# Optimization experiments

Measured on AMD Instinct MI355X. Metric: run time of the kernel, lower is better.

## Reference

```python
import jax, jax.numpy as jnp
import numpy as np

N_USERS = 100000
N_ITEMS = 50000
N_NODES = N_USERS + N_ITEMS
EMB = 64
N_LAYERS = 2
N_EDGES = 4000000
LN_EPS = 1e-5


def setup_inputs() -> dict:
    key = jax.random.key(0)
    ks = jax.random.split(key, 16)
    d = {}
    d['user_emb'] = jax.random.normal(ks[0], (N_USERS, EMB), jnp.float32) * 0.1
    d['item_emb'] = jax.random.normal(ks[1], (N_ITEMS, EMB), jnp.float32) * 0.1
    d['modal_feat0'] = jax.random.normal(ks[2], (N_ITEMS, 768), jnp.float32)
    d['modal_feat1'] = jax.random.normal(ks[3], (N_ITEMS, 384), jnp.float32)
    d['modal_feat2'] = jax.random.normal(ks[4], (N_USERS, 128), jnp.float32)
    for m, fdim in enumerate([768, 384, 128]):
        d[f'enc_W{m}'] = jax.random.normal(ks[5 + m], (fdim, EMB), jnp.float32) / np.sqrt(fdim)
        d[f'enc_b{m}'] = jnp.zeros((EMB,), jnp.float32)
        d[f'enc_g{m}'] = jnp.ones((EMB,), jnp.float32)
        d[f'enc_be{m}'] = jnp.zeros((EMB,), jnp.float32)
    d['attn_W1'] = jax.random.normal(ks[8], (2 * EMB, EMB), jnp.float32) / np.sqrt(2 * EMB)
    d['attn_b1'] = jnp.zeros((EMB,), jnp.float32)
    d['attn_W2'] = jax.random.normal(ks[9], (EMB, 3), jnp.float32) / np.sqrt(EMB)
    d['attn_b2'] = jnp.zeros((3,), jnp.float32)
    # symmetric-normalized-ish positive edge weights, COO edge list
    d['adj_vals'] = jax.random.uniform(ks[10], (N_EDGES,), jnp.float32) * 0.05
    d['adj_rows'] = jax.random.randint(ks[11], (N_EDGES,), 0, N_NODES, jnp.int32)
    d['adj_cols'] = jax.random.randint(ks[12], (N_EDGES,), 0, N_NODES, jnp.int32)
    return d


def _layernorm(h, g, b):
    mu = h.mean(-1, keepdims=True)
    var = ((h - mu) ** 2).mean(-1, keepdims=True)
    return (h - mu) * jax.lax.rsqrt(var + LN_EPS) * g + b


def _encode(x, W, b, g, be):
    # Linear -> LayerNorm -> LeakyReLU(0.2); Dropout is identity at inference
    return jax.nn.leaky_relu(_layernorm(x @ W + b, g, be), 0.2)


def reference(user_emb, item_emb, modal_feat0, modal_feat1, modal_feat2,
              enc_W0, enc_b0, enc_g0, enc_be0,
              enc_W1, enc_b1, enc_g1, enc_be1,
              enc_W2, enc_b2, enc_g2, enc_be2,
              attn_W1, attn_b1, attn_W2, attn_b2,
              adj_vals, adj_rows, adj_cols):
    # item-level modalities
    m0 = _encode(modal_feat0, enc_W0, enc_b0, enc_g0, enc_be0)        # [I, D]
    m1 = _encode(modal_feat1, enc_W1, enc_b1, enc_g1, enc_be1)        # [I, D]
    # user-level modality: mean over users, broadcast to items
    um = _encode(modal_feat2, enc_W2, enc_b2, enc_g2, enc_be2)        # [U, D]
    m2 = jnp.broadcast_to(um.mean(0, keepdims=True), (N_ITEMS, EMB))  # [I, D]
    item_modal = jnp.stack([m0, m1, m2], axis=1)                      # [I, 3, D]

    # modal attention from (mean user emb, item emb)
    u_mean = jnp.broadcast_to(user_emb.mean(0, keepdims=True), (N_ITEMS, EMB))
    att_in = jnp.concatenate([u_mean, item_emb], axis=1)              # [I, 2D]
    w = jax.nn.softmax(jnp.tanh(att_in @ attn_W1 + attn_b1) @ attn_W2 + attn_b2, axis=-1)  # [I, 3]
    item_weighted = jnp.einsum('imd,im->id', item_modal, w)

    all_emb = jnp.concatenate([user_emb, item_emb + item_weighted], axis=0)  # [N, D]

    def spmm(e):
        return jax.ops.segment_sum(adj_vals[:, None] * e[adj_cols], adj_rows,
                                   num_segments=N_NODES)

    acc = all_emb
    e = all_emb
    for _ in range(N_LAYERS):
        e = spmm(e)
        acc = acc + e
    out = acc / (N_LAYERS + 1)
    return out[:N_USERS], out[N_USERS:]
```

## Files before the change

kernel.cpp:

```cpp
#include <hip/hip_runtime.h>
#include <cstdint>

#define N_USERS 100000
#define N_ITEMS 50000
#define N_NODES (N_USERS + N_ITEMS)
#define EMB 64
#define N_EDGES 4000000
#define LN_EPS 1e-5f

#define NBKT 586
#define C_BLOCKS 1024
#define EPB 3907
#define BCAP 7680
#define ENC128_BLOCKS 1563
#define ENC_ITEM_BLOCKS 782
#define UPREP_BLOCKS 512

#define K1_SMEM 37056

__device__ __forceinline__ float b2f(unsigned short h) {
    return __uint_as_float((unsigned)h << 16);
}
__device__ __forceinline__ unsigned short f2b(float f) {
    unsigned u = __float_as_uint(f);
    u += 0x7FFFu + ((u >> 16) & 1u);
    return (unsigned short)(u >> 16);
}
__device__ __forceinline__ uint2 pack4(float a, float b, float c, float d) {
    return make_uint2((unsigned)f2b(a) | ((unsigned)f2b(b) << 16),
                      (unsigned)f2b(c) | ((unsigned)f2b(d) << 16));
}

template<int WRITE_OUT>
__device__ __forceinline__ void enc_body(
    int blk, char* smem, const float* __restrict__ X, const float* __restrict__ W,
    const float* __restrict__ bb, const float* __restrict__ gg,
    const float* __restrict__ be, float* __restrict__ out,
    float* __restrict__ colsum, int K, int R)
{
    float (*sXT)[68] = reinterpret_cast<float(*)[68]>(smem);
    float (*sW)[64] = reinterpret_cast<float(*)[64]>(smem + 8704);
    float* scs = reinterpret_cast<float*>(smem + 8704 + 8192);

    int tid = threadIdx.x;
    int tx = tid & 15;
    int ty = tid >> 4;
    int rbase = blk * 64;

    int xr = tid >> 2;
    int xc = (tid & 3) * 8;
    int wr = tid >> 3;
    int wc = (tid & 7) * 8;

    int gxrow = rbase + xr; if (gxrow >= R) gxrow = R - 1;
    const float* xsrc = X + (size_t)gxrow * K + xc;

    float4 bv = *reinterpret_cast<const float4*>(&bb[tx * 4]);
    float4 gv = *reinterpret_cast<const float4*>(&gg[tx * 4]);
    float4 bev = *reinterpret_cast<const float4*>(&be[tx * 4]);

    float acc[4][4];
    #pragma unroll
    for (int i = 0; i < 4; ++i) {
        acc[i][0] = bv.x; acc[i][1] = bv.y; acc[i][2] = bv.z; acc[i][3] = bv.w;
    }

    for (int kc = 0; kc < K; kc += 32) {
        float4 a0 = *reinterpret_cast<const float4*>(xsrc + kc);
        float4 a1 = *reinterpret_cast<const float4*>(xsrc + kc + 4);
        float4 w0 = *reinterpret_cast<const float4*>(&W[(size_t)(kc + wr) * EMB + wc]);
        float4 w1 = *reinterpret_cast<const float4*>(&W[(size_t)(kc + wr) * EMB + wc + 4]);
        __syncthreads();
        sXT[xc + 0][xr] = a0.x; sXT[xc + 1][xr] = a0.y;
        sXT[xc + 2][xr] = a0.z; sXT[xc + 3][xr] = a0.w;
        sXT[xc + 4][xr] = a1.x; sXT[xc + 5][xr] = a1.y;
        sXT[xc + 6][xr] = a1.z; sXT[xc + 7][xr] = a1.w;
        *reinterpret_cast<float4*>(&sW[wr][wc]) = w0;
        *reinterpret_cast<float4*>(&sW[wr][wc + 4]) = w1;
        __syncthreads();
        #pragma unroll
        for (int k = 0; k < 32; ++k) {
            float4 xv = *reinterpret_cast<const float4*>(&sXT[k][ty * 4]);
            float4 wv = *reinterpret_cast<const float4*>(&sW[k][tx * 4]);
            float xs[4] = {xv.x, xv.y, xv.z, xv.w};
            float wsv[4] = {wv.x, wv.y, wv.z, wv.w};
            #pragma unroll
            for (int i = 0; i < 4; ++i)
                #pragma unroll
                for (int j = 0; j < 4; ++j)
                    acc[i][j] = fmaf(xs[i], wsv[j], acc[i][j]);
        }
    }

    float gls[4] = {gv.x, gv.y, gv.z, gv.w};
    float bels[4] = {bev.x, bev.y, bev.z, bev.w};
    float csum[4] = {0.f, 0.f, 0.f, 0.f};
    #pragma unroll
    for (int i = 0; i < 4; ++i) {
        float s = acc[i][0] + acc[i][1] + acc[i][2] + acc[i][3];
        float q = acc[i][0]*acc[i][0] + acc[i][1]*acc[i][1]
                + acc[i][2]*acc[i][2] + acc[i][3]*acc[i][3];
        #pragma unroll
        for (int off = 1; off < 16; off <<= 1) {
            s += __shfl_xor(s, off, 64);
            q += __shfl_xor(q, off, 64);
        }
        float mu = s * (1.f / EMB);
        float var = q * (1.f / EMB) - mu * mu;
        float rs = rsqrtf(var + LN_EPS);
        int row = rbase + ty * 4 + i;
        bool valid = row < R;
        float t[4];
        #pragma unroll
        for (int j = 0; j < 4; ++j) {
            float v = (acc[i][j] - mu) * rs * gls[j] + bels[j];
            t[j] = v > 0.f ? v : 0.2f * v;
        }
        if (WRITE_OUT) {
            if (valid)
                *reinterpret_cast<float4*>(&out[(size_t)row * EMB + tx * 4]) =
                    make_float4(t[0], t[1], t[2], t[3]);
        } else {
            #pragma unroll
            for (int j = 0; j < 4; ++j) csum[j] += valid ? t[j] : 0.f;
        }
    }

    if (!WRITE_OUT) {
        #pragma unroll
        for (int j = 0; j < 4; ++j) {
            csum[j] += __shfl_xor(csum[j], 16, 64);
            csum[j] += __shfl_xor(csum[j], 32, 64);
        }
        if (tid < 64) scs[tid] = 0.f;
        __syncthreads();
        if ((tid & 63) < 16) {
            #pragma unroll
            for (int j = 0; j < 4; ++j) atomicAdd(&scs[tx * 4 + j], csum[j]);
        }
        __syncthreads();
        if (tid < 64) unsafeAtomicAdd(&colsum[tid], scs[tid]);
    }
}

__device__ __forceinline__ void scatter_sort_body(
    int blk, char* smem, const int* __restrict__ rows,
    const int* __restrict__ cols, const float* __restrict__ vals,
    int* __restrict__ bktcnt, int* __restrict__ hmatT, int2* __restrict__ tmp)
{
    int2* stage = reinterpret_cast<int2*>(smem);
    int* cnt = reinterpret_cast<int*>(smem + 31264);
    int* offA = reinterpret_cast<int*>(smem + 31264 + 2344);
    int* sums = reinterpret_cast<int*>(smem + 31264 + 2344 + 2348);

    int tid = threadIdx.x;
    int s = blk * EPB;
    int e = s + EPB; if (e > N_EDGES) e = N_EDGES;
    int n = e - s;

    for (int i = tid; i < NBKT; i += 256) cnt[i] = 0;
    __syncthreads();
    for (int i = s + tid; i < e; i += 256)
        atomicAdd(&cnt[rows[i] >> 8], 1);
    __syncthreads();

    int base = tid * 3;
    int loc[3]; int run = 0;
    #pragma unroll
    for (int j = 0; j < 3; ++j) {
        int idx = base + j;
        int v = (idx < NBKT) ? cnt[idx] : 0;
        loc[j] = run; run += v;
    }
    sums[tid] = run;
    __syncthreads();
    for (int off = 1; off < 256; off <<= 1) {
        int u = (tid >= off) ? sums[tid - off] : 0;
        __syncthreads();
        sums[tid] += u;
        __syncthreads();
    }
    int excl = tid ? sums[tid - 1] : 0;
    #pragma unroll
    for (int j = 0; j < 3; ++j) {
        int idx = base + j;
        if (idx < NBKT) offA[idx] = excl + loc[j];
    }
    if (tid == 0) offA[NBKT] = n;
    __syncthreads();

    for (int i = tid; i < NBKT; i += 256) {
        if (cnt[i]) atomicAdd(&bktcnt[i], cnt[i]);
        cnt[i] = offA[i];
    }
    for (int i = tid; i <= NBKT; i += 256)
        hmatT[i * C_BLOCKS + blk] = offA[i];
    __syncthreads();

    for (int i = s + tid; i < e; i += 256) {
        int r = rows[i];
        int p = atomicAdd(&cnt[r >> 8], 1);
        stage[p] = make_int2(cols[i] | ((r & 255) << 18), __float_as_int(vals[i]));
    }
    __syncthreads();

    int2* dst = tmp + (size_t)blk * EPB;
    for (int i = tid; i < n; i += 256) dst[i] = stage[i];
}

__device__ __forceinline__ void user_prep_body(
    int bid, int nblk, char* smem, const float* __restrict__ U,
    float* __restrict__ e0, unsigned short* __restrict__ e0b,
    float* __restrict__ sum)
{
    float* scs = reinterpret_cast<float*>(smem);
    int tid = threadIdx.x;
    int lane = tid & 63;
    const int n4 = N_USERS * EMB / 4;
    int stride = nblk * 256;
    const float4* A = reinterpret_cast<const float4*>(U);
    float4* O = reinterpret_cast<float4*>(e0);
    uint2* OB = reinterpret_cast<uint2*>(e0b);
    float c0 = 0.f, c1 = 0.f, c2 = 0.f, c3 = 0.f;
    for (int i = bid * 256 + tid; i < n4; i += stride) {
        float4 v = A[i];
        O[i] = v;
        OB[i] = pack4(v.x, v.y, v.z, v.w);
        c0 += v.x; c1 += v.y; c2 += v.z; c3 += v.w;
    }
    c0 += __shfl_xor(c0, 16, 64); c0 += __shfl_xor(c0, 32, 64);
    c1 += __shfl_xor(c1, 16, 64); c1 += __shfl_xor(c1, 32, 64);
    c2 += __shfl_xor(c2, 16, 64); c2 += __shfl_xor(c2, 32, 64);
    c3 += __shfl_xor(c3, 16, 64); c3 += __shfl_xor(c3, 32, 64);
    if (tid < 64) scs[tid] = 0.f;
    __syncthreads();
    if (lane < 16) {
        atomicAdd(&scs[lane * 4 + 0], c0);
        atomicAdd(&scs[lane * 4 + 1], c1);
        atomicAdd(&scs[lane * 4 + 2], c2);
        atomicAdd(&scs[lane * 4 + 3], c3);
    }
    __syncthreads();
    if (tid < 64) unsafeAtomicAdd(&sum[tid], scs[tid]);
}

__global__ __launch_bounds__(256) void k1_kernel(
    const int* __restrict__ rows, const int* __restrict__ cols,
    const float* __restrict__ vals, int* __restrict__ bktcnt,
    int* __restrict__ hmatT, int2* __restrict__ tmp,
    const float* __restrict__ mf2, const float* __restrict__ W2,
    const float* __restrict__ b2v, const float* __restrict__ g2,
    const float* __restrict__ be2, float* __restrict__ hdr)
{
    extern __shared__ char smem[];
    int bid = blockIdx.x;
    if (bid < C_BLOCKS)
        scatter_sort_body(bid, smem, rows, cols, vals, bktcnt, hmatT, tmp);
    else
        enc_body<0>(bid - C_BLOCKS, smem, mf2, W2, b2v, g2, be2,
                    nullptr, hdr + 64, 128, N_USERS);
}

__global__ __launch_bounds__(256) void k3_kernel(
    const float* __restrict__ mf0, const float* __restrict__ W0,
    const float* __restrict__ b0v, const float* __restrict__ g0,
    const float* __restrict__ be0, float* __restrict__ m0b,
    const float* __restrict__ mf1, const float* __restrict__ W1,
    const float* __restrict__ b1v, const float* __restrict__ g1,
    const float* __restrict__ be1, float* __restrict__ m1b,
    const float* __restrict__ U, float* __restrict__ e0,
    unsigned short* __restrict__ e0b, float* __restrict__ hdr)
{
    __shared__ __align__(16) char smem[17152];
    int bid = blockIdx.x;
    if (bid < ENC_ITEM_BLOCKS)
        enc_body<1>(bid, smem, mf0, W0, b0v, g0, be0, m0b, nullptr, 768, N_ITEMS);
    else if (bid < 2 * ENC_ITEM_BLOCKS)
        enc_body<1>(bid - ENC_ITEM_BLOCKS, smem, mf1, W1, b1v, g1, be1, m1b,
                    nullptr, 384, N_ITEMS);
    else
        user_prep_body(bid - 2 * ENC_ITEM_BLOCKS, UPREP_BLOCKS, smem, U, e0, e0b, hdr);
}

__global__ void finalize_kernel(const float* __restrict__ aW1,
                                const float* __restrict__ ab1,
                                float* __restrict__ hdr)
{
    int d = threadIdx.x;
    float um = hdr[d] * (1.f / N_USERS);
    float m2 = hdr[64 + d] * (1.f / N_USERS);
    hdr[128 + d] = um;
    hdr[192 + d] = m2;
    float acc = ab1[d];
    for (int k = 0; k < EMB; ++k)
        acc = fmaf(hdr[k] * (1.f / N_USERS), aW1[k * EMB + d], acc);
    hdr[256 + d] = acc;
}

__global__ __launch_bounds__(256) void item_fuse_gemm_kernel(
    const float* __restrict__ item_emb, const float* __restrict__ m0,
    const float* __restrict__ m1, const float* __restrict__ hdr,
    const float* __restrict__ aW1, const float* __restrict__ aW2,
    const float* __restrict__ ab2, float* __restrict__ e0,
    unsigned short* __restrict__ e0b)
{
    __shared__ float sIE[64][68];
    __shared__ float sW1[64][64];

    int tid = threadIdx.x;
    int tx = tid & 15;
    int ty = tid >> 4;
    int rbase = blockIdx.x * 64;

    int lr = tid >> 2;
    int lc = (tid & 3) * 16;
    int grow = rbase + lr; if (grow >= N_ITEMS) grow = N_ITEMS - 1;
    const float4* ier = reinterpret_cast<const float4*>(item_emb + (size_t)grow * EMB + lc);
    const float4* wsrc = reinterpret_cast<const float4*>(aW1 + (size_t)(64 + lr) * EMB + lc);
    #pragma unroll
    for (int q = 0; q < 4; ++q) {
        float4 v = ier[q];
        sIE[lc + q*4 + 0][lr] = v.x; sIE[lc + q*4 + 1][lr] = v.y;
        sIE[lc + q*4 + 2][lr] = v.z; sIE[lc + q*4 + 3][lr] = v.w;
        *reinterpret_cast<float4*>(&sW1[lr][lc + q*4]) = wsrc[q];
    }
    __syncthreads();

    float4 pre = *reinterpret_cast<const float4*>(&hdr[256 + tx * 4]);
    float acc[4][4];
    #pragma unroll
    for (int i = 0; i < 4; ++i) {
        acc[i][0] = pre.x; acc[i][1] = pre.y; acc[i][2] = pre.z; acc[i][3] = pre.w;
    }
    #pragma unroll 8
    for (int k = 0; k < 64; ++k) {
        float4 xv = *reinterpret_cast<const float4*>(&sIE[k][ty * 4]);
        float4 wv = *reinterpret_cast<const float4*>(&sW1[k][tx * 4]);
        float xs[4] = {xv.x, xv.y, xv.z, xv.w};
        float wsv[4] = {wv.x, wv.y, wv.z, wv.w};
        #pragma unroll
        for (int i = 0; i < 4; ++i)
            #pragma unroll
            for (int j = 0; j < 4; ++j)
                acc[i][j] = fmaf(xs[i], wsv[j], acc[i][j]);
    }

    float aw[4][3];
    #pragma unroll
    for (int j = 0; j < 4; ++j) {
        aw[j][0] = aW2[(tx*4 + j)*3 + 0];
        aw[j][1] = aW2[(tx*4 + j)*3 + 1];
        aw[j][2] = aW2[(tx*4 + j)*3 + 2];
    }
    float sc[4][3];
    #pragma unroll
    for (int i = 0; i < 4; ++i) { sc[i][0] = 0.f; sc[i][1] = 0.f; sc[i][2] = 0.f; }
    #pragma unroll
    for (int i = 0; i < 4; ++i)
        #pragma unroll
        for (int j = 0; j < 4; ++j) {
            float t = tanhf(acc[i][j]);
            sc[i][0] = fmaf(t, aw[j][0], sc[i][0]);
            sc[i][1] = fmaf(t, aw[j][1], sc[i][1]);
            sc[i][2] = fmaf(t, aw[j][2], sc[i][2]);
        }
    #pragma unroll
    for (int i = 0; i < 4; ++i)
        #pragma unroll
        for (int r = 0; r < 3; ++r) {
            float v = sc[i][r];
            #pragma unroll
            for (int off = 1; off < 16; off <<= 1) v += __shfl_xor(v, off, 64);
            sc[i][r] = v;
        }

    float b20 = ab2[0], b21 = ab2[1], b22 = ab2[2];
    float4 m2v = *reinterpret_cast<const float4*>(&hdr[192 + tx * 4]);
    float m2s[4] = {m2v.x, m2v.y, m2v.z, m2v.w};

    #pragma unroll
    for (int i = 0; i < 4; ++i) {
        int row = rbase + ty * 4 + i;
        if (row >= N_ITEMS) break;
        float s0 = sc[i][0] + b20, s1 = sc[i][1] + b21, s2 = sc[i][2] + b22;
        float mx = fmaxf(s0, fmaxf(s1, s2));
        float e0w = expf(s0 - mx), e1w = expf(s1 - mx), e2w = expf(s2 - mx);
        float inv = 1.f / (e0w + e1w + e2w);
        float w0 = e0w * inv, w1 = e1w * inv, w2 = e2w * inv;

        float4 a = *reinterpret_cast<const float4*>(&m0[(size_t)row * EMB + tx * 4]);
        float4 bq = *reinterpret_cast<const float4*>(&m1[(size_t)row * EMB + tx * 4]);
        int lrow = ty * 4 + i;
        float res[4];
        #pragma unroll
        for (int j = 0; j < 4; ++j) {
            float ie = sIE[tx * 4 + j][lrow];
            float mm = (j == 0 ? a.x : j == 1 ? a.y : j == 2 ? a.z : a.w);
            float m1e = (j == 0 ? bq.x : j == 1 ? bq.y : j == 2 ? bq.z : bq.w);
            res[j] = ie + w0 * mm + w1 * m1e + w2 * m2s[j];
        }
        size_t idx = (size_t)(N_USERS + row) * EMB + tx * 4;
        *reinterpret_cast<float4*>(&e0[idx]) = make_float4(res[0], res[1], res[2], res[3]);
        *reinterpret_cast<uint2*>(&e0b[idx]) = pack4(res[0], res[1], res[2], res[3]);
    }
}

__global__ __launch_bounds__(256) void gather_csr_kernel(
    const int2* __restrict__ tmp, const int* __restrict__ hmatT,
    const int* __restrict__ bktcnt, int* __restrict__ offs,
    int2* __restrict__ edges)
{
    __shared__ int cnt[256], pos[256], sbk[256];
    __shared__ int2 stage[BCAP];
    int b = blockIdx.x;
    int t = threadIdx.x;

    int base = t * 3, part = 0;
    #pragma unroll
    for (int j = 0; j < 3; ++j) {
        int idx = base + j;
        if (idx < b) part += bktcnt[idx];
    }
    sbk[t] = part;
    cnt[t] = 0;
    __syncthreads();
    for (int off = 1; off < 256; off <<= 1) {
        int u = (t >= off) ? sbk[t - off] : 0;
        __syncthreads();
        sbk[t] += u;
        __syncthreads();
    }
    int gb = sbk[255];

    const int* h0 = hmatT + (size_t)b * C_BLOCKS;
    const int* h1 = hmatT + (size_t)(b + 1) * C_BLOCKS;

    for (int blk = t; blk < C_BLOCKS; blk += 256) {
        int st = h0[blk], en = h1[blk];
        const int2* src = tmp + (size_t)blk * EPB;
        for (int i = st; i < en; ++i)
            atomicAdd(&cnt[(src[i].x >> 18) & 255], 1);
    }
    __syncthreads();

    int v = cnt[t];
    __syncthreads();
    for (int off = 1; off < 256; off <<= 1) {
        int u = (t >= off) ? cnt[t - off] : 0;
        __syncthreads();
        cnt[t] += u;
        __syncthreads();
    }
    int incl = cnt[t];
    int row = (b << 8) + t;
    if (row < N_NODES) offs[row] = gb + incl;
    pos[t] = incl - v;
    __syncthreads();
    int total = cnt[255];
    if (total > BCAP) total = BCAP;

    for (int blk = t; blk < C_BLOCKS; blk += 256) {
        int st = h0[blk], en = h1[blk];
        const int2* src = tmp + (size_t)blk * EPB;
        for (int i = st; i < en; ++i) {
            int2 ed = src[i];
            int p = atomicAdd(&pos[(ed.x >> 18) & 255], 1);
            if (p < BCAP)
                stage[p] = make_int2(ed.x & 0x3FFFF, ed.y);
        }
    }
    __syncthreads();

    for (int i = t; i < total; i += 256)
        edges[gb + i] = stage[i];
}

template<int FINAL>
__global__ __launch_bounds__(256) void spmm_csr_kernel(
    const int* __restrict__ offs, const int2* __restrict__ edges,
    const unsigned short* __restrict__ srcb, const float* __restrict__ e0f,
    float* __restrict__ outf, unsigned short* __restrict__ dstb)
{
    int r = __builtin_amdgcn_readfirstlane(blockIdx.x * 4 + (threadIdx.x >> 6));
    if (r >= N_NODES) return;
    int d = threadIdx.x & 63;
    int start = __builtin_amdgcn_readfirstlane((r == 0) ? 0 : offs[r - 1]);
    int end = __builtin_amdgcn_readfirstlane(offs[r]);
    const unsigned long long* ep = reinterpret_cast<const unsigned long long*>(edges);

    float a0 = 0.f, a1 = 0.f, a2 = 0.f, a3 = 0.f;
    int i = start;
    for (; i + 8 <= end; i += 8) {
        unsigned long long q0 = __builtin_nontemporal_load(ep + i + 0);
        unsigned long long q1 = __builtin_nontemporal_load(ep + i + 1);
        unsigned long long q2 = __builtin_nontemporal_load(ep + i + 2);
        unsigned long long q3 = __builtin_nontemporal_load(ep + i + 3);
        unsigned long long q4 = __builtin_nontemporal_load(ep + i + 4);
        unsigned long long q5 = __builtin_nontemporal_load(ep + i + 5);
        unsigned long long q6 = __builtin_nontemporal_load(ep + i + 6);
        unsigned long long q7 = __builtin_nontemporal_load(ep + i + 7);
        float x0 = b2f(srcb[(size_t)(unsigned)q0 * EMB + d]);
        float x1 = b2f(srcb[(size_t)(unsigned)q1 * EMB + d]);
        float x2 = b2f(srcb[(size_t)(unsigned)q2 * EMB + d]);
        float x3 = b2f(srcb[(size_t)(unsigned)q3 * EMB + d]);
        float x4 = b2f(srcb[(size_t)(unsigned)q4 * EMB + d]);
        float x5 = b2f(srcb[(size_t)(unsigned)q5 * EMB + d]);
        float x6 = b2f(srcb[(size_t)(unsigned)q6 * EMB + d]);
        float x7 = b2f(srcb[(size_t)(unsigned)q7 * EMB + d]);
        a0 = fmaf(__uint_as_float((unsigned)(q0 >> 32)), x0, a0);
        a1 = fmaf(__uint_as_float((unsigned)(q1 >> 32)), x1, a1);
        a2 = fmaf(__uint_as_float((unsigned)(q2 >> 32)), x2, a2);
        a3 = fmaf(__uint_as_float((unsigned)(q3 >> 32)), x3, a3);
        a0 = fmaf(__uint_as_float((unsigned)(q4 >> 32)), x4, a0);
        a1 = fmaf(__uint_as_float((unsigned)(q5 >> 32)), x5, a1);
        a2 = fmaf(__uint_as_float((unsigned)(q6 >> 32)), x6, a2);
        a3 = fmaf(__uint_as_float((unsigned)(q7 >> 32)), x7, a3);
    }
    for (; i < end; ++i) {
        unsigned long long q = __builtin_nontemporal_load(ep + i);
        float x = b2f(srcb[(size_t)(unsigned)q * EMB + d]);
        a0 = fmaf(__uint_as_float((unsigned)(q >> 32)), x, a0);
    }
    float s = (a0 + a1) + (a2 + a3);
    size_t idx = (size_t)r * EMB + d;
    if (FINAL) {
        float add = e0f[idx] + b2f(srcb[idx]);
        __builtin_nontemporal_store((add + s) * (1.f / 3.f), &outf[idx]);
    } else {
        dstb[idx] = f2b(s);
    }
}

extern "C" void kernel_launch(void* const* d_in, const int* in_sizes, int n_in,
                              void* d_out, int out_size, void* d_ws, size_t ws_size,
                              hipStream_t stream)
{
    const float* user_emb = (const float*)d_in[0];
    const float* item_emb = (const float*)d_in[1];
    const float* mf0 = (const float*)d_in[2];
    const float* mf1 = (const float*)d_in[3];
    const float* mf2 = (const float*)d_in[4];
    const float* W0  = (const float*)d_in[5];
    const float* b0  = (const float*)d_in[6];
    const float* g0  = (const float*)d_in[7];
    const float* be0 = (const float*)d_in[8];
    const float* W1  = (const float*)d_in[9];
    const float* b1  = (const float*)d_in[10];
    const float* g1  = (const float*)d_in[11];
    const float* be1 = (const float*)d_in[12];
    const float* W2  = (const float*)d_in[13];
    const float* b2  = (const float*)d_in[14];
    const float* g2  = (const float*)d_in[15];
    const float* be2 = (const float*)d_in[16];
    const float* aW1 = (const float*)d_in[17];
    const float* ab1 = (const float*)d_in[18];
    const float* aW2 = (const float*)d_in[19];
    const float* ab2 = (const float*)d_in[20];
    const float* avals = (const float*)d_in[21];
    const int* arows = (const int*)d_in[22];
    const int* acols = (const int*)d_in[23];
    float* out = (float*)d_out;

    float* ws  = (float*)d_ws;
    float* hdr = ws;
    int*   bktcnt = (int*)(ws + 512);
    float* m0b = ws + 1152;
    float* m1b = m0b + (size_t)N_ITEMS * EMB;
    float* e0  = m1b + (size_t)N_ITEMS * EMB;
    unsigned short* e0b = (unsigned short*)(e0 + (size_t)N_NODES * EMB);
    unsigned short* e1b = e0b + (size_t)N_NODES * EMB;
    int*   offs = (int*)(e1b + (size_t)N_NODES * EMB);
    int2*  edges = (int2*)(offs + N_NODES);
    int2*  tmp = (int2*)e0;
    int*   hmatT = (int*)m0b;

    hipMemsetAsync(hdr, 0, 4608, stream);

    k1_kernel<<<C_BLOCKS + ENC128_BLOCKS, 256, K1_SMEM, stream>>>(
        arows, acols, avals, bktcnt, hmatT, tmp, mf2, W2, b2, g2, be2, hdr);
    gather_csr_kernel<<<NBKT, 256, 0, stream>>>(tmp, hmatT, bktcnt, offs, edges);
    k3_kernel<<<2 * ENC_ITEM_BLOCKS + UPREP_BLOCKS, 256, 0, stream>>>(
        mf0, W0, b0, g0, be0, m0b, mf1, W1, b1, g1, be1, m1b,
        user_emb, e0, e0b, hdr);
    finalize_kernel<<<1, 64, 0, stream>>>(aW1, ab1, hdr);
    item_fuse_gemm_kernel<<<ENC_ITEM_BLOCKS, 256, 0, stream>>>(
        item_emb, m0b, m1b, hdr, aW1, aW2, ab2, e0, e0b);

    spmm_csr_kernel<0><<<(N_NODES + 3) / 4, 256, 0, stream>>>(
        offs, edges, e0b, nullptr, nullptr, e1b);
    spmm_csr_kernel<1><<<(N_NODES + 3) / 4, 256, 0, stream>>>(
        offs, edges, e1b, e0, out, nullptr);
}
```

Before: 538.7 us.

## Fuse CSR gather into encoder kernel with finer buckets; drop fp32 e0 copy

Halves the row-bucket width (256 to 128 rows, 1172 buckets) so each gather block stages fewer edges and uses less shared memory. The gather step then runs as extra blocks of the item-encoder/user-prep kernel, which saves one launch and lets the two overlap. The fp32 copy of the layer-0 embedding is removed, and the final layer reads the bf16 copy instead, cutting write and read traffic. The risks are a small precision loss in the final sum, since the e0 term is now rounded to bf16, and more hmatT traffic from the doubled bucket count. The workspace is relaid so tmp and hmatT no longer alias buffers that the fused kernel writes.

Result: faster. 490.7 us (-8.9%).

```diff
diff --git a/kernel.cpp b/kernel.cpp
--- a/kernel.cpp
+++ b/kernel.cpp
@@ -8,15 +8,16 @@
 #define N_EDGES 4000000
 #define LN_EPS 1e-5f
 
-#define NBKT 586
+#define NBKT 1172
 #define C_BLOCKS 1024
 #define EPB 3907
-#define BCAP 7680
+#define BCAP 4096
 #define ENC128_BLOCKS 1563
 #define ENC_ITEM_BLOCKS 782
 #define UPREP_BLOCKS 512
 
-#define K1_SMEM 37056
+#define K1_SMEM 41728
+#define K2_SMEM 35840
 
 __device__ __forceinline__ float b2f(unsigned short h) {
     return __uint_as_float((unsigned)h << 16);
@@ -149,9 +150,9 @@
     int* __restrict__ bktcnt, int* __restrict__ hmatT, int2* __restrict__ tmp)
 {
     int2* stage = reinterpret_cast<int2*>(smem);
-    int* cnt = reinterpret_cast<int*>(smem + 31264);
-    int* offA = reinterpret_cast<int*>(smem + 31264 + 2344);
-    int* sums = reinterpret_cast<int*>(smem + 31264 + 2344 + 2348);
+    int* cnt  = reinterpret_cast<int*>(smem + 31264);
+    int* offA = reinterpret_cast<int*>(smem + 35952);
+    int* sums = reinterpret_cast<int*>(smem + 40656);
 
     int tid = threadIdx.x;
     int s = blk * EPB;
@@ -161,13 +162,13 @@
     for (int i = tid; i < NBKT; i += 256) cnt[i] = 0;
     __syncthreads();
     for (int i = s + tid; i < e; i += 256)
-        atomicAdd(&cnt[rows[i] >> 8], 1);
-    __syncthreads();
-
-    int base = tid * 3;
-    int loc[3]; int run = 0;
-    #pragma unroll
-    for (int j = 0; j < 3; ++j) {
+        atomicAdd(&cnt[rows[i] >> 7], 1);
+    __syncthreads();
+
+    int base = tid * 5;
+    int loc[5]; int run = 0;
+    #pragma unroll
+    for (int j = 0; j < 5; ++j) {
         int idx = base + j;
         int v = (idx < NBKT) ? cnt[idx] : 0;
         loc[j] = run; run += v;
@@ -182,7 +183,7 @@
     }
     int excl = tid ? sums[tid - 1] : 0;
     #pragma unroll
-    for (int j = 0; j < 3; ++j) {
+    for (int j = 0; j < 5; ++j) {
         int idx = base + j;
         if (idx < NBKT) offA[idx] = excl + loc[j];
     }
@@ -194,13 +195,13 @@
         cnt[i] = offA[i];
     }
     for (int i = tid; i <= NBKT; i += 256)
-        hmatT[i * C_BLOCKS + blk] = offA[i];
+        hmatT[(size_t)i * C_BLOCKS + blk] = offA[i];
     __syncthreads();
 
     for (int i = s + tid; i < e; i += 256) {
         int r = rows[i];
-        int p = atomicAdd(&cnt[r >> 8], 1);
-        stage[p] = make_int2(cols[i] | ((r & 255) << 18), __float_as_int(vals[i]));
+        int p = atomicAdd(&cnt[r >> 7], 1);
+        stage[p] = make_int2(cols[i] | ((r & 127) << 18), __float_as_int(vals[i]));
     }
     __syncthreads();
 
@@ -208,10 +209,80 @@
     for (int i = tid; i < n; i += 256) dst[i] = stage[i];
 }
 
+__device__ __forceinline__ void gather_body(
+    int b, char* smem, const int2* __restrict__ tmp,
+    const int* __restrict__ hmatT, const int* __restrict__ bktcnt,
+    int* __restrict__ offs, int2* __restrict__ edges)
+{
+    int2* stage = reinterpret_cast<int2*>(smem);
+    int* cnt = reinterpret_cast<int*>(smem + 32768);
+    int* pos = reinterpret_cast<int*>(smem + 33792);
+    int* sbk = reinterpret_cast<int*>(smem + 34816);
+    int t = threadIdx.x;
+
+    int base = t * 5, part = 0;
+    #pragma unroll
+    for (int j = 0; j < 5; ++j) {
+        int idx = base + j;
+        if (idx < b) part += bktcnt[idx];
+    }
+    sbk[t] = part;
+    cnt[t] = 0;
+    __syncthreads();
+    for (int off = 1; off < 256; off <<= 1) {
+        int u = (t >= off) ? sbk[t - off] : 0;
+        __syncthreads();
+        sbk[t] += u;
+        __syncthreads();
+    }
+    int gb = sbk[255];
+
+    const int* h0 = hmatT + (size_t)b * C_BLOCKS;
+    const int* h1 = hmatT + (size_t)(b + 1) * C_BLOCKS;
+
+    for (int blk = t; blk < C_BLOCKS; blk += 256) {
+        int st = h0[blk], en = h1[blk];
+        const int2* src = tmp + (size_t)blk * EPB;
+        for (int i = st; i < en; ++i)
+            atomicAdd(&cnt[(src[i].x >> 18) & 127], 1);
+    }
+    __syncthreads();
+
+    int v = cnt[t];
+    __syncthreads();
+    for (int off = 1; off < 256; off <<= 1) {
+        int u = (t >= off) ? cnt[t - off] : 0;
+        __syncthreads();
+        cnt[t] += u;
+        __syncthreads();
+    }
+    int incl = cnt[t];
+    int row = (b << 7) + t;
+    if (t < 128 && row < N_NODES) offs[row] = gb + incl;
+    pos[t] = incl - v;
+    __syncthreads();
+    int total = cnt[255];
+    if (total > BCAP) total = BCAP;
+
+    for (int blk = t; blk < C_BLOCKS; blk += 256) {
+        int st = h0[blk], en = h1[blk];
+        const int2* src = tmp + (size_t)blk * EPB;
+        for (int i = st; i < en; ++i) {
+            int2 ed = src[i];
+            int p = atomicAdd(&pos[(ed.x >> 18) & 127], 1);
+            if (p < BCAP)
+                stage[p] = make_int2(ed.x & 0x3FFFF, ed.y);
+        }
+    }
+    __syncthreads();
+
+    for (int i = t; i < total; i += 256)
+        edges[gb + i] = stage[i];
+}
+
 __device__ __forceinline__ void user_prep_body(
     int bid, int nblk, char* smem, const float* __restrict__ U,
-    float* __restrict__ e0, unsigned short* __restrict__ e0b,
-    float* __restrict__ sum)
+    unsigned short* __restrict__ e0b, float* __restrict__ sum)
 {
     float* scs = reinterpret_cast<float*>(smem);
     int tid = threadIdx.x;
@@ -219,12 +290,10 @@
     const int n4 = N_USERS * EMB / 4;
     int stride = nblk * 256;
     const float4* A = reinterpret_cast<const float4*>(U);
-    float4* O = reinterpret_cast<float4*>(e0);
     uint2* OB = reinterpret_cast<uint2*>(e0b);
     float c0 = 0.f, c1 = 0.f, c2 = 0.f, c3 = 0.f;
     for (int i = bid * 256 + tid; i < n4; i += stride) {
         float4 v = A[i];
-        O[i] = v;
         OB[i] = pack4(v.x, v.y, v.z, v.w);
         c0 += v.x; c1 += v.y; c2 += v.z; c3 += v.w;
     }
@@ -261,25 +330,32 @@
                     nullptr, hdr + 64, 128, N_USERS);
 }
 
-__global__ __launch_bounds__(256) void k3_kernel(
+__global__ __launch_bounds__(256) void k2_kernel(
+    const int2* __restrict__ tmp, const int* __restrict__ hmatT,
+    const int* __restrict__ bktcnt, int* __restrict__ offs,
+    int2* __restrict__ edges,
     const float* __restrict__ mf0, const float* __restrict__ W0,
     const float* __restrict__ b0v, const float* __restrict__ g0,
     const float* __restrict__ be0, float* __restrict__ m0b,
     const float* __restrict__ mf1, const float* __restrict__ W1,
     const float* __restrict__ b1v, const float* __restrict__ g1,
     const float* __restrict__ be1, float* __restrict__ m1b,
-    const float* __restrict__ U, float* __restrict__ e0,
-    unsigned short* __restrict__ e0b, float* __restrict__ hdr)
-{
-    __shared__ __align__(16) char smem[17152];
+    const float* __restrict__ U, unsigned short* __restrict__ e0b,
+    float* __restrict__ hdr)
+{
+    extern __shared__ char smem[];
     int bid = blockIdx.x;
-    if (bid < ENC_ITEM_BLOCKS)
-        enc_body<1>(bid, smem, mf0, W0, b0v, g0, be0, m0b, nullptr, 768, N_ITEMS);
-    else if (bid < 2 * ENC_ITEM_BLOCKS)
-        enc_body<1>(bid - ENC_ITEM_BLOCKS, smem, mf1, W1, b1v, g1, be1, m1b,
-                    nullptr, 384, N_ITEMS);
+    if (bid < NBKT)
+        gather_body(bid, smem, tmp, hmatT, bktcnt, offs, edges);
+    else if (bid < NBKT + ENC_ITEM_BLOCKS)
+        enc_body<1>(bid - NBKT, smem, mf0, W0, b0v, g0, be0, m0b,
+                    nullptr, 768, N_ITEMS);
+    else if (bid < NBKT + 2 * ENC_ITEM_BLOCKS)
+        enc_body<1>(bid - NBKT - ENC_ITEM_BLOCKS, smem, mf1, W1, b1v, g1, be1,
+                    m1b, nullptr, 384, N_ITEMS);
     else
-        user_prep_body(bid - 2 * ENC_ITEM_BLOCKS, UPREP_BLOCKS, smem, U, e0, e0b, hdr);
+        user_prep_body(bid - NBKT - 2 * ENC_ITEM_BLOCKS, UPREP_BLOCKS, smem,
+                       U, e0b, hdr);
 }
 
 __global__ void finalize_kernel(const float* __restrict__ aW1,
@@ -301,8 +377,7 @@
     const float* __restrict__ item_emb, const float* __restrict__ m0,
     const float* __restrict__ m1, const float* __restrict__ hdr,
     const float* __restrict__ aW1, const float* __restrict__ aW2,
-    const float* __restrict__ ab2, float* __restrict__ e0,
-    unsigned short* __restrict__ e0b)
+    const float* __restrict__ ab2, unsigned short* __restrict__ e0b)
 {
     __shared__ float sIE[64][68];
     __shared__ float sW1[64][64];
@@ -400,85 +475,14 @@
             res[j] = ie + w0 * mm + w1 * m1e + w2 * m2s[j];
         }
         size_t idx = (size_t)(N_USERS + row) * EMB + tx * 4;
-        *reinterpret_cast<float4*>(&e0[idx]) = make_float4(res[0], res[1], res[2], res[3]);
         *reinterpret_cast<uint2*>(&e0b[idx]) = pack4(res[0], res[1], res[2], res[3]);
     }
-}
-
-__global__ __launch_bounds__(256) void gather_csr_kernel(
-    const int2* __restrict__ tmp, const int* __restrict__ hmatT,
-    const int* __restrict__ bktcnt, int* __restrict__ offs,
-    int2* __restrict__ edges)
-{
-    __shared__ int cnt[256], pos[256], sbk[256];
-    __shared__ int2 stage[BCAP];
-    int b = blockIdx.x;
-    int t = threadIdx.x;
-
-    int base = t * 3, part = 0;
-    #pragma unroll
-    for (int j = 0; j < 3; ++j) {
-        int idx = base + j;
-        if (idx < b) part += bktcnt[idx];
-    }
-    sbk[t] = part;
-    cnt[t] = 0;
-    __syncthreads();
-    for (int off = 1; off < 256; off <<= 1) {
-        int u = (t >= off) ? sbk[t - off] : 0;
-        __syncthreads();
-        sbk[t] += u;
-        __syncthreads();
-    }
-    int gb = sbk[255];
-
-    const int* h0 = hmatT + (size_t)b * C_BLOCKS;
-    const int* h1 = hmatT + (size_t)(b + 1) * C_BLOCKS;
-
-    for (int blk = t; blk < C_BLOCKS; blk += 256) {
-        int st = h0[blk], en = h1[blk];
-        const int2* src = tmp + (size_t)blk * EPB;
-        for (int i = st; i < en; ++i)
-            atomicAdd(&cnt[(src[i].x >> 18) & 255], 1);
-    }
-    __syncthreads();
-
-    int v = cnt[t];
-    __syncthreads();
-    for (int off = 1; off < 256; off <<= 1) {
-        int u = (t >= off) ? cnt[t - off] : 0;
-        __syncthreads();
-        cnt[t] += u;
-        __syncthreads();
-    }
-    int incl = cnt[t];
-    int row = (b << 8) + t;
-    if (row < N_NODES) offs[row] = gb + incl;
-    pos[t] = incl - v;
-    __syncthreads();
-    int total = cnt[255];
-    if (total > BCAP) total = BCAP;
-
-    for (int blk = t; blk < C_BLOCKS; blk += 256) {
-        int st = h0[blk], en = h1[blk];
-        const int2* src = tmp + (size_t)blk * EPB;
-        for (int i = st; i < en; ++i) {
-            int2 ed = src[i];
-            int p = atomicAdd(&pos[(ed.x >> 18) & 255], 1);
-            if (p < BCAP)
-                stage[p] = make_int2(ed.x & 0x3FFFF, ed.y);
-        }
-    }
-    __syncthreads();
-
-    for (int i = t; i < total; i += 256)
-        edges[gb + i] = stage[i];
 }
 
 template<int FINAL>
 __global__ __launch_bounds__(256) void spmm_csr_kernel(
     const int* __restrict__ offs, const int2* __restrict__ edges,
-    const unsigned short* __restrict__ srcb, const float* __restrict__ e0f,
+    const unsigned short* __restrict__ srcb, const unsigned short* __restrict__ e0bm,
     float* __restrict__ outf, unsigned short* __restrict__ dstb)
 {
     int r = __builtin_amdgcn_readfirstlane(blockIdx.x * 4 + (threadIdx.x >> 6));
@@ -524,7 +528,7 @@
     float s = (a0 + a1) + (a2 + a3);
     size_t idx = (size_t)r * EMB + d;
     if (FINAL) {
-        float add = e0f[idx] + b2f(srcb[idx]);
+        float add = b2f(e0bm[idx]) + b2f(srcb[idx]);
         __builtin_nontemporal_store((add + s) * (1.f / 3.f), &outf[idx]);
     } else {
         dstb[idx] = f2b(s);
@@ -564,30 +568,29 @@
     float* ws  = (float*)d_ws;
     float* hdr = ws;
     int*   bktcnt = (int*)(ws + 512);
-    float* m0b = ws + 1152;
+    float* m0b = ws + 1792;
     float* m1b = m0b + (size_t)N_ITEMS * EMB;
-    float* e0  = m1b + (size_t)N_ITEMS * EMB;
-    unsigned short* e0b = (unsigned short*)(e0 + (size_t)N_NODES * EMB);
+    unsigned short* e0b = (unsigned short*)(m1b + (size_t)N_ITEMS * EMB);
     unsigned short* e1b = e0b + (size_t)N_NODES * EMB;
     int*   offs = (int*)(e1b + (size_t)N_NODES * EMB);
     int2*  edges = (int2*)(offs + N_NODES);
-    int2*  tmp = (int2*)e0;
-    int*   hmatT = (int*)m0b;
-
-    hipMemsetAsync(hdr, 0, 4608, stream);
+    int2*  tmp = edges + N_EDGES;
+    int*   hmatT = (int*)(tmp + N_EDGES);
+
+    hipMemsetAsync(hdr, 0, 2048 + NBKT * 4, stream);
 
     k1_kernel<<<C_BLOCKS + ENC128_BLOCKS, 256, K1_SMEM, stream>>>(
         arows, acols, avals, bktcnt, hmatT, tmp, mf2, W2, b2, g2, be2, hdr);
-    gather_csr_kernel<<<NBKT, 256, 0, stream>>>(tmp, hmatT, bktcnt, offs, edges);
-    k3_kernel<<<2 * ENC_ITEM_BLOCKS + UPREP_BLOCKS, 256, 0, stream>>>(
+    k2_kernel<<<NBKT + 2 * ENC_ITEM_BLOCKS + UPREP_BLOCKS, 256, K2_SMEM, stream>>>(
+        tmp, hmatT, bktcnt, offs, edges,
         mf0, W0, b0, g0, be0, m0b, mf1, W1, b1, g1, be1, m1b,
-        user_emb, e0, e0b, hdr);
+        user_emb, e0b, hdr);
     finalize_kernel<<<1, 64, 0, stream>>>(aW1, ab1, hdr);
     item_fuse_gemm_kernel<<<ENC_ITEM_BLOCKS, 256, 0, stream>>>(
-        item_emb, m0b, m1b, hdr, aW1, aW2, ab2, e0, e0b);
+        item_emb, m0b, m1b, hdr, aW1, aW2, ab2, e0b);
 
     spmm_csr_kernel<0><<<(N_NODES + 3) / 4, 256, 0, stream>>>(
         offs, edges, e0b, nullptr, nullptr, e1b);
     spmm_csr_kernel<1><<<(N_NODES + 3) / 4, 256, 0, stream>>>(
-        offs, edges, e1b, e0, out, nullptr);
-}
+        offs, edges, e1b, e0b, out, nullptr);
+}
```
